# Performance work log

Hardware: AMD Instinct MI355X
Metric: run time of the kernel (lower is better)

Reference implementation:

```python
import jax, jax.numpy as jnp
import numpy as np

H = 1024      # hidden_size
V = 32000     # vocab_size
MAX_LEN = 32  # decode steps
B = 64        # batch


def _uni(key, shape, s):
    return jax.random.uniform(key, shape, jnp.float32, -s, s)


def setup_inputs() -> dict:
    key = jax.random.key(0)
    ks = jax.random.split(key, 10)
    s = 1.0 / np.sqrt(H)
    return {
        "vectors": jax.random.normal(ks[0], (B, H), jnp.float32),
        "W_fc_in": _uni(ks[1], (H, H), s),
        "b_fc_in": _uni(ks[2], (H,), s),
        "W_ih": _uni(ks[3], (3 * H, H), s),   # torch GRU weight_ih_l0 (r,z,n)
        "W_hh": _uni(ks[4], (3 * H, H), s),
        "b_ih": _uni(ks[5], (3 * H,), s),
        "b_hh": _uni(ks[6], (3 * H,), s),
        "W_out": _uni(ks[7], (V, H), s),
        "b_out": _uni(ks[8], (V,), s),
        "top_k": 8,
    }


def reference(vectors, W_fc_in, b_fc_in, W_ih, W_hh, b_ih, b_hh, W_out, b_out, top_k):
    # hidden = fc_in(vectors); initial GRU input is zeros
    h0 = vectors @ W_fc_in.T + b_fc_in           # [B, H]
    x0 = jnp.zeros_like(h0)

    def gru_cell(carry, _):
        h, x = carry
        gi = x @ W_ih.T + b_ih                   # [B, 3H]
        gh = h @ W_hh.T + b_hh                   # [B, 3H]
        i_r, i_z, i_n = jnp.split(gi, 3, axis=-1)
        h_r, h_z, h_n = jnp.split(gh, 3, axis=-1)
        r = jax.nn.sigmoid(i_r + h_r)
        z = jax.nn.sigmoid(i_z + h_z)
        n = jnp.tanh(i_n + r * h_n)
        h_new = (1.0 - z) * n + z * h            # PyTorch GRU update
        # out == h_new for single-layer GRU; inputs = out feeds back
        return (h_new, h_new), h_new

    _, outs = jax.lax.scan(gru_cell, (h0, x0), None, length=MAX_LEN)  # [T, B, H]

    # fc_out + log_softmax over vocab, for all steps at once
    logits = jnp.einsum('tbh,vh->tbv', outs, W_out) + b_out           # [T, B, V]
    logp = jax.nn.log_softmax(logits, axis=-1)

    # topk then multinomial over exp(top logp) == categorical over top logp
    top_p, top_i = jax.lax.top_k(logp, top_k)                         # [T, B, K]
    samp = jax.random.categorical(jax.random.key(42), top_p, axis=-1)  # [T, B]
    tokens = jnp.take_along_axis(top_i, samp[..., None], axis=-1)[..., 0]
    return tokens.T.astype(jnp.int32)                                  # [B, T]
```

## Files before the change

### kernel.cpp

```cpp
#include <hip/hip_runtime.h>
#include <stdint.h>

typedef unsigned int u32;
typedef unsigned long long u64;
typedef unsigned short ushort;
typedef __attribute__((ext_vector_type(8))) short bf16x8;
typedef __attribute__((ext_vector_type(4))) float f32x4;

#define JAX_PARTITIONABLE 1

#define HD     1024
#define BBATCH 64
#define TSTEP  32
#define VOCAB  32000
#define NROWS  2048
#define GATE6  6144
#define NCB    250
#define NCAND  16

__device__ __forceinline__ void threefry2x32(u32 k0, u32 k1, u32 x0, u32 x1,
                                             u32& y0, u32& y1) {
  u32 ks2 = k0 ^ k1 ^ 0x1BD11BDAu;
  x0 += k0; x1 += k1;
#define TFR(r) do { x0 += x1; x1 = (x1 << (r)) | (x1 >> (32 - (r))); x1 ^= x0; } while (0)
  TFR(13); TFR(15); TFR(26); TFR(6);   x0 += k1;  x1 += ks2 + 1u;
  TFR(17); TFR(29); TFR(16); TFR(24);  x0 += ks2; x1 += k0 + 2u;
  TFR(13); TFR(15); TFR(26); TFR(6);   x0 += k0;  x1 += k1 + 3u;
  TFR(17); TFR(29); TFR(16); TFR(24);  x0 += k1;  x1 += ks2 + 4u;
  TFR(13); TFR(15); TFR(26); TFR(6);   x0 += ks2; x1 += k0 + 5u;
#undef TFR
  y0 = x0; y1 = x1;
}

__device__ __forceinline__ u32 jax_random_bits(u32 n) {
#if JAX_PARTITIONABLE
  u32 y0, y1; threefry2x32(0u, 42u, 0u, n, y0, y1);
  return y0 ^ y1;
#else
  u32 y0, y1;
  if (n < 8192u) { threefry2x32(0u, 42u, n, n + 8192u, y0, y1); return y0; }
  else           { threefry2x32(0u, 42u, n - 8192u, n, y0, y1); return y1; }
#endif
}

__device__ __forceinline__ u64 packkey(float v, int idx) {
  u32 b = __float_as_uint(v);
  b = (b & 0x80000000u) ? ~b : (b | 0x80000000u);
  return ((u64)b << 32) | (u64)(~(u32)idx);
}

__device__ __forceinline__ void insert4(u64* t4, u64 k) {
  if (k > t4[3]) {
    t4[3] = k;
    if (t4[3] > t4[2]) { u64 tm = t4[2]; t4[2] = t4[3]; t4[3] = tm; }
    if (t4[2] > t4[1]) { u64 tm = t4[1]; t4[1] = t4[2]; t4[2] = tm; }
    if (t4[1] > t4[0]) { u64 tm = t4[0]; t4[0] = t4[1]; t4[1] = tm; }
  }
}

__device__ __forceinline__ ushort f2bf_rne(float x) {
  u32 u = __float_as_uint(x);
  return (ushort)((u + 0x7fffu + ((u >> 16) & 1u)) >> 16);
}
__device__ __forceinline__ float bf2f(ushort h) {
  return __uint_as_float(((u32)h) << 16);
}

typedef const __attribute__((address_space(1))) void* gas_ptr;
typedef __attribute__((address_space(3))) void* las_ptr;
__device__ __forceinline__ void gload16(const void* g, void* l) {
  __builtin_amdgcn_global_load_lds((gas_ptr)g, (las_ptr)l, 16, 0, 0);
}

__global__ __launch_bounds__(256) void tobf16(const float* __restrict__ src,
                                              ushort* __restrict__ dst, int n8) {
  int i = blockIdx.x * 256 + threadIdx.x;
  const int stride = gridDim.x * 256;
  for (; i < n8; i += stride) {
    const float4* s4 = (const float4*)src + (size_t)i * 2;
    float4 a = s4[0], b = s4[1];
    u32 o0 = f2bf_rne(a.x) | ((u32)f2bf_rne(a.y) << 16);
    u32 o1 = f2bf_rne(a.z) | ((u32)f2bf_rne(a.w) << 16);
    u32 o2 = f2bf_rne(b.x) | ((u32)f2bf_rne(b.y) << 16);
    u32 o3 = f2bf_rne(b.z) | ((u32)f2bf_rne(b.w) << 16);
    ((uint4*)dst)[i] = make_uint4(o0, o1, o2, o3);
  }
}

__global__ __launch_bounds__(256) void tobf16x3_gruP(
    const float* __restrict__ Wih, const float* __restrict__ Whh,
    ushort* __restrict__ w1, ushort* __restrict__ w2, ushort* __restrict__ w3) {
  int i = blockIdx.x * 256 + threadIdx.x;
  if (i >= GATE6 * (HD / 8)) return;
  int rp = i >> 7;
  int kc = i & 127;
  int b = rp / 48, rem = rp % 48;
  int g = rem >> 3, jp = rem & 7;
  const float* src = (g < 3)
      ? (Wih + ((size_t)g * HD + b * 8 + jp) * HD)
      : (Whh + ((size_t)(g - 3) * HD + b * 8 + jp) * HD);
  const float4* s4 = (const float4*)(src + kc * 8);
  float v[8];
  float4 a = s4[0], bb = s4[1];
  v[0]=a.x; v[1]=a.y; v[2]=a.z; v[3]=a.w; v[4]=bb.x; v[5]=bb.y; v[6]=bb.z; v[7]=bb.w;
  ushort p1[8], p2[8], p3[8];
#pragma unroll
  for (int e = 0; e < 8; ++e) {
    p1[e] = f2bf_rne(v[e]);
    float r1 = v[e] - bf2f(p1[e]);
    p2[e] = f2bf_rne(r1);
    float r2 = r1 - bf2f(p2[e]);
    p3[e] = f2bf_rne(r2);
  }
  u32 o1[4], o2[4], o3[4];
#pragma unroll
  for (int e = 0; e < 4; ++e) {
    o1[e] = p1[2*e] | ((u32)p1[2*e+1] << 16);
    o2[e] = p2[2*e] | ((u32)p2[2*e+1] << 16);
    o3[e] = p3[2*e] | ((u32)p3[2*e+1] << 16);
  }
  ((uint4*)w1)[i] = make_uint4(o1[0], o1[1], o1[2], o1[3]);
  ((uint4*)w2)[i] = make_uint4(o2[0], o2[1], o2[2], o2[3]);
  ((uint4*)w3)[i] = make_uint4(o3[0], o3[1], o3[2], o3[3]);
}

__global__ __launch_bounds__(256) void gemm64_nt(
    const float* __restrict__ A, const float* __restrict__ B,
    float* __restrict__ part) {
  __shared__ float4 As4[64 * 33];
  __shared__ float4 Bs4[32 * 33];
  const int tid = threadIdx.x;
  const int n0 = blockIdx.x * 32;
  const float* Brow = B + (size_t)n0 * HD;
  const int ks = blockIdx.y * 256;
  const int tc = tid & 7, trg = tid >> 3;
  float acc[2][4] = {};
  for (int kc = 0; kc < 2; ++kc) {
    const int k0 = ks + kc * 128;
#pragma unroll
    for (int l = 0; l < 8; ++l) {
      int m = tid + l * 256; int row = m >> 5, k4 = m & 31;
      As4[row * 33 + k4] = *(const float4*)(A + (size_t)row * HD + k0 + k4 * 4);
    }
#pragma unroll
    for (int l = 0; l < 4; ++l) {
      int m = tid + l * 256; int row = m >> 5, k4 = m & 31;
      Bs4[row * 33 + k4] = *(const float4*)(Brow + (size_t)row * HD + k0 + k4 * 4);
    }
    __syncthreads();
#pragma unroll
    for (int kq = 0; kq < 32; ++kq) {
      float4 av[2], bv[4];
      av[0] = As4[trg * 33 + kq];
      av[1] = As4[(trg + 32) * 33 + kq];
      bv[0] = Bs4[tc * 33 + kq];
      bv[1] = Bs4[(tc + 8) * 33 + kq];
      bv[2] = Bs4[(tc + 16) * 33 + kq];
      bv[3] = Bs4[(tc + 24) * 33 + kq];
#pragma unroll
      for (int i = 0; i < 2; ++i)
#pragma unroll
        for (int j = 0; j < 4; ++j) {
          acc[i][j] += av[i].x * bv[j].x;
          acc[i][j] += av[i].y * bv[j].y;
          acc[i][j] += av[i].z * bv[j].z;
          acc[i][j] += av[i].w * bv[j].w;
        }
    }
    __syncthreads();
  }
  float* P = part + (size_t)blockIdx.y * BBATCH * HD;
#pragma unroll
  for (int i = 0; i < 2; ++i) {
    int b = trg + 32 * i;
#pragma unroll
    for (int j = 0; j < 4; ++j)
      P[(size_t)b * HD + n0 + tc + 8 * j] = acc[i][j];
  }
}

__global__ __launch_bounds__(256) void combine_fcin(
    const float* __restrict__ part, const float* __restrict__ b_fc,
    float* __restrict__ h, ushort* __restrict__ h1, ushort* __restrict__ h2,
    ushort* __restrict__ h3) {
  int idx = blockIdx.x * 256 + threadIdx.x;
  int j = idx & 1023; int b = idx >> 10;
  const size_t S = (size_t)BBATCH * HD;
  const float* p = part + (size_t)b * HD;
  float d = p[j]; d += p[S + j]; d += p[2 * S + j]; d += p[3 * S + j];
  float hv = d + b_fc[j];
  h[idx] = hv;
  ushort a = f2bf_rne(hv);
  float r1 = hv - bf2f(a);
  ushort bb = f2bf_rne(r1);
  float r2 = r1 - bf2f(bb);
  h1[idx] = a; h2[idx] = bb; h3[idx] = f2bf_rne(r2);
}

__global__ __launch_bounds__(128) void gru_step(
    const ushort* __restrict__ W1, const ushort* __restrict__ W2,
    const ushort* __restrict__ W3,
    const float* __restrict__ b_ih, const float* __restrict__ b_hh,
    float* __restrict__ h, float* __restrict__ outs,
    ushort* __restrict__ outs_bf,
    ushort* __restrict__ h1, ushort* __restrict__ h2, ushort* __restrict__ h3,
    int t) {
  __shared__ ushort Bs[2][3][3072];
  const int tid = threadIdx.x;
  const int lane = tid & 63, w = tid >> 6;
  const int grp = blockIdx.x >> 4;
  const int rmd = blockIdx.x & 15;
  const int hb = rmd >> 3;
  const int b = grp * 8 + (rmd & 7);
  const ushort* B1g = W1 + (size_t)b * 48 * HD;
  const ushort* B2g = W2 + (size_t)b * 48 * HD;
  const ushort* B3g = W3 + (size_t)b * 48 * HD;
  const int rc = lane >> 3;
  const int gr8 = ((lane & 7) ^ rc) * 8;
  const int l15 = lane & 15;
  const int kc4 = lane >> 4;
  const int arow = hb * 32 + w * 16 + l15;

#define STAGE_B(buf, kt) do {                                         \
    const int k0_ = (kt) * 64;                                        \
    _Pragma("unroll")                                                 \
    for (int c_ = 0; c_ < 9; ++c_) {                                  \
      int q_ = w * 9 + c_;                                            \
      const ushort* src_; ushort* dst_;                               \
      if (q_ < 6)       { src_ = B1g + (size_t)(q_ * 8 + rc) * HD;    \
                          dst_ = &Bs[buf][0][q_ * 512]; }             \
      else if (q_ < 12) { src_ = B2g + (size_t)((q_ - 6) * 8 + rc) * HD; \
                          dst_ = &Bs[buf][1][(q_ - 6) * 512]; }       \
      else              { src_ = B3g + (size_t)((q_ - 12) * 8 + rc) * HD; \
                          dst_ = &Bs[buf][2][(q_ - 12) * 512]; }      \
      gload16(src_ + k0_ + gr8, dst_);                                \
    }                                                                 \
  } while (0)

#define LOAD_A(dst, kt) do {                                          \
    _Pragma("unroll")                                                 \
    for (int ks_ = 0; ks_ < 2; ++ks_) {                               \
      const int ke_ = (kt) * 64 + ks_ * 32 + kc4 * 8;                 \
      dst[ks_][0] = *(const bf16x8*)(h1 + (size_t)arow * HD + ke_);   \
      dst[ks_][1] = *(const bf16x8*)(h2 + (size_t)arow * HD + ke_);   \
      dst[ks_][2] = *(const bf16x8*)(h3 + (size_t)arow * HD + ke_);   \
    }                                                                 \
  } while (0)

#define COMPUTE_G(AR, buf) do {                                       \
    _Pragma("unroll")                                                 \
    for (int ks_ = 0; ks_ < 2; ++ks_) {                               \
      const int kb_ = ks_ * 64 + kc4 * 16;                            \
      bf16x8 b1_[3], b2_[3], b3_[3];                                  \
      _Pragma("unroll")                                               \
      for (int nt_ = 0; nt_ < 3; ++nt_) {                             \
        int br_ = nt_ * 16 + l15;                                     \
        int bo_ = br_ * 128 + (kb_ ^ ((br_ & 7) << 4));               \
        b1_[nt_] = *(const bf16x8*)((const char*)&Bs[buf][0][0] + bo_); \
        b2_[nt_] = *(const bf16x8*)((const char*)&Bs[buf][1][0] + bo_); \
        b3_[nt_] = *(const bf16x8*)((const char*)&Bs[buf][2][0] + bo_); \
      }                                                               \
      _Pragma("unroll")                                               \
      for (int nt_ = 0; nt_ < 3; ++nt_) {                             \
        acc[nt_] = __builtin_amdgcn_mfma_f32_16x16x32_bf16(AR[ks_][2], b1_[nt_], acc[nt_], 0, 0, 0); \
        acc[nt_] = __builtin_amdgcn_mfma_f32_16x16x32_bf16(AR[ks_][0], b3_[nt_], acc[nt_], 0, 0, 0); \
        acc[nt_] = __builtin_amdgcn_mfma_f32_16x16x32_bf16(AR[ks_][1], b2_[nt_], acc[nt_], 0, 0, 0); \
        acc[nt_] = __builtin_amdgcn_mfma_f32_16x16x32_bf16(AR[ks_][1], b1_[nt_], acc[nt_], 0, 0, 0); \
        acc[nt_] = __builtin_amdgcn_mfma_f32_16x16x32_bf16(AR[ks_][0], b2_[nt_], acc[nt_], 0, 0, 0); \
        acc[nt_] = __builtin_amdgcn_mfma_f32_16x16x32_bf16(AR[ks_][0], b1_[nt_], acc[nt_], 0, 0, 0); \
      }                                                               \
    }                                                                 \
  } while (0)

  f32x4 acc[3];
#pragma unroll
  for (int nt = 0; nt < 3; ++nt) acc[nt] = (f32x4){0.f, 0.f, 0.f, 0.f};

  bf16x8 aA[2][3], aB[2][3];
  LOAD_A(aA, 0); STAGE_B(0, 0);
  LOAD_A(aB, 1); STAGE_B(1, 1);

#pragma unroll
  for (int kt2 = 0; kt2 < 8; ++kt2) {
    const int kte = kt2 * 2, kto = kte + 1;
    asm volatile("s_waitcnt vmcnt(15)" ::: "memory");
    __builtin_amdgcn_s_barrier();
    __builtin_amdgcn_sched_barrier(0);
    COMPUTE_G(aA, 0);
    __builtin_amdgcn_sched_barrier(0);
    __builtin_amdgcn_s_barrier();
    if (kte + 2 < 16) { LOAD_A(aA, kte + 2); STAGE_B(0, kte + 2); }
    if (kto < 15) {
      asm volatile("s_waitcnt vmcnt(15)" ::: "memory");
    } else {
      asm volatile("s_waitcnt vmcnt(0)" ::: "memory");
    }
    __builtin_amdgcn_s_barrier();
    __builtin_amdgcn_sched_barrier(0);
    COMPUTE_G(aB, 1);
    __builtin_amdgcn_sched_barrier(0);
    __builtin_amdgcn_s_barrier();
    if (kto + 2 < 16) { LOAD_A(aB, kto + 2); STAGE_B(1, kto + 2); }
  }
#undef STAGE_B
#undef LOAD_A
#undef COMPUTE_G

  const bool low = (l15 < 8);
  const int j = b * 8 + l15;
  float bi_r = 0.f, bi_z = 0.f, bi_n = 0.f, bh_r = 0.f, bh_z = 0.f, bh_n = 0.f;
  if (low) {
    bi_r = b_ih[j]; bi_z = b_ih[HD + j]; bi_n = b_ih[2 * HD + j];
    bh_r = b_hh[j]; bh_z = b_hh[HD + j]; bh_n = b_hh[2 * HD + j];
  }
#pragma unroll
  for (int r = 0; r < 4; ++r) {
    float v0 = acc[0][r], v1 = acc[1][r], v2 = acc[2][r];
    float p0 = __shfl_xor(v0, 8);
    float p1 = __shfl_xor(v1, 8);
    float p2 = __shfl_xor(v2, 8);
    if (low) {
      float gir = (t == 0) ? bi_r : (v0 + bi_r);
      float giz = (t == 0) ? bi_z : (p0 + bi_z);
      float gin = (t == 0) ? bi_n : (v1 + bi_n);
      float ghr = p1 + bh_r;
      float ghz = v2 + bh_z;
      float ghn = p2 + bh_n;
      float rr = 1.0f / (1.0f + expf(-(gir + ghr)));
      float zz = 1.0f / (1.0f + expf(-(giz + ghz)));
      float nn = tanhf(gin + rr * ghn);
      int i = hb * 32 + w * 16 + (lane >> 4) * 4 + r;
      int idx = i * HD + j;
      float hp = h[idx];
      float hn2 = (1.0f - zz) * nn + zz * hp;
      h[idx] = hn2;
      size_t o = ((size_t)t * BBATCH + i) * HD + j;
      outs[o] = hn2;
      ushort a = f2bf_rne(hn2);
      outs_bf[o] = a;
      float r1 = hn2 - bf2f(a);
      ushort bb2 = f2bf_rne(r1);
      float r2 = r1 - bf2f(bb2);
      h1[idx] = a; h2[idx] = bb2; h3[idx] = f2bf_rne(r2);
    }
  }
}

__global__ __launch_bounds__(256) void gemm_out_mfma(
    const ushort* __restrict__ Abf, const ushort* __restrict__ Bbf,
    const float* __restrict__ b_out, u64* __restrict__ keys) {
  __shared__ ushort Sm[2][2][8192];
  float* Cs = (float*)&Sm[0][0][0];
  u64* pkL1 = (u64*)((char*)&Sm[0][0][0] + 17024);
  u64* pkL2 = pkL1 + 1024;

  const int tid = threadIdx.x;
  const int lane = tid & 63;
  const int wid = tid >> 6;
  const int wr = wid >> 1, wc = wid & 1;
  const int cb = blockIdx.y;
  const int n0 = cb * 128;
  const int r0 = blockIdx.x * 128;

  const ushort* Ag = Abf + (size_t)r0 * HD;
  const ushort* Bg = Bbf + (size_t)n0 * HD;
  const int rc = lane >> 3;
  const int gr8 = ((lane & 7) ^ rc) * 8;
  const int l15 = lane & 15;
  const int kseg = (lane >> 4) * 16;

#define STAGE_OUT(buf, kt) do {                                      \
    ushort* SA_ = &Sm[buf][0][0];                                    \
    ushort* SB_ = &Sm[buf][1][0];                                    \
    const int k0_ = (kt) * 64;                                       \
    _Pragma("unroll")                                                \
    for (int c_ = 0; c_ < 4; ++c_) {                                 \
      int ch_ = wid * 4 + c_;                                        \
      int row_ = ch_ * 8 + rc;                                       \
      gload16(Ag + (size_t)row_ * HD + k0_ + gr8, SA_ + ch_ * 512);  \
      gload16(Bg + (size_t)row_ * HD + k0_ + gr8, SB_ + ch_ * 512);  \
    }                                                                \
  } while (0)

#define COMPUTE_OUT(buf) do {                                        \
    const ushort* SA_ = &Sm[buf][0][0];                              \
    const ushort* SB_ = &Sm[buf][1][0];                              \
    _Pragma("unroll")                                                \
    for (int ks_ = 0; ks_ < 2; ++ks_) {                              \
      bf16x8 a_[4], b_[4];                                           \
      const int kb_ = ks_ * 64 + kseg;                               \
      _Pragma("unroll")                                              \
      for (int m_ = 0; m_ < 4; ++m_) {                               \
        int row_ = wr * 64 + m_ * 16 + l15;                          \
        int off_ = row_ * 128 + (kb_ ^ ((row_ & 7) << 4));           \
        a_[m_] = *(const bf16x8*)((const char*)SA_ + off_);          \
// ... 30 lines not shown
      STAGE_OUT(p ^ 1, kt + 1);
      asm volatile("s_waitcnt vmcnt(8)" ::: "memory");
    } else {
      asm volatile("s_waitcnt vmcnt(0)" ::: "memory");
    }
    __builtin_amdgcn_s_barrier();
    __builtin_amdgcn_sched_barrier(0);
    COMPUTE_OUT(p);
    __builtin_amdgcn_sched_barrier(0);
    __builtin_amdgcn_s_barrier();
    p ^= 1;
  }
  __syncthreads();

#pragma unroll
  for (int q = 0; q < 4; ++q) {
    if (wr == (q >> 1)) {
#pragma unroll
      for (int mi = 0; mi < 2; ++mi) {
        const int m = (q & 1) * 2 + mi;
#pragma unroll
        for (int n = 0; n < 4; ++n) {
          int c = wc * 64 + n * 16 + l15;
#pragma unroll
          for (int j = 0; j < 4; ++j) {
            int lr = mi * 16 + (lane >> 4) * 4 + j;
            Cs[lr * 133 + c] = acc[m][n][j] + bo[n];
          }
        }
      }
    }
    __syncthreads();
    {
      int rr = tid >> 3, seg = tid & 7;
      const float* rp = Cs + rr * 133 + seg * 16;
      u64 t4[4] = {0, 0, 0, 0};
#pragma unroll
      for (int c = 0; c < 16; ++c) insert4(t4, packkey(rp[c], n0 + seg * 16 + c));
      u64* d = pkL1 + (rr * 8 + seg) * 4;
      d[0] = t4[0]; d[1] = t4[1]; d[2] = t4[2]; d[3] = t4[3];
    }
    __syncthreads();
    if (tid < 64) {
      int rr = tid >> 1, hf = tid & 1;
      const u64* s = pkL1 + (rr * 8 + hf * 4) * 4;
      u64 t4[4] = {s[0], s[1], s[2], s[3]};
#pragma unroll
      for (int e = 4; e < 16; ++e) insert4(t4, s[e]);
      u64* d = pkL2 + tid * 4;
      d[0] = t4[0]; d[1] = t4[1]; d[2] = t4[2]; d[3] = t4[3];
    }
    __syncthreads();
    if (tid < 32) {
      const u64* s = pkL2 + tid * 8;
      u64 t4[4] = {s[0], s[1], s[2], s[3]};
      insert4(t4, s[4]); insert4(t4, s[5]); insert4(t4, s[6]); insert4(t4, s[7]);
      int grow = r0 + q * 32 + tid;
      u64* kp2 = keys + ((size_t)grow * NCB + cb) * 4;
      kp2[0] = t4[0]; kp2[1] = t4[1]; kp2[2] = t4[2]; kp2[3] = t4[3];
    }
    __syncthreads();
  }
#undef STAGE_OUT
#undef COMPUTE_OUT
}

__global__ __launch_bounds__(64) void merge_sample2(
// ... 87 lines not shown
      u32 bits = jax_random_bits((u32)(r * 8 + k));
      float f = __uint_as_float((bits >> 9) | 0x3f800000u) - 1.0f;
      float u = f * (1.0f - TINY) + TINY;
      u = fmaxf(TINY, u);
      float g = -logf(-logf(u));
      float s = g + lp;
      if (s > best) { best = s; bi = k; }
    }
    int t = r >> 6, b = r & 63;
    out[b * TSTEP + t] = vi[bi];
  }
}

extern "C" void kernel_launch(void* const* d_in, const int* in_sizes, int n_in,
                              void* d_out, int out_size, void* d_ws, size_t ws_size,
                              hipStream_t stream) {
  (void)in_sizes; (void)n_in; (void)out_size; (void)ws_size;
  const float* vectors = (const float*)d_in[0];
  const float* W_fc_in = (const float*)d_in[1];
  const float* b_fc_in = (const float*)d_in[2];
  const float* W_ih    = (const float*)d_in[3];
  const float* W_hh    = (const float*)d_in[4];
  const float* b_ih    = (const float*)d_in[5];
  const float* b_hh    = (const float*)d_in[6];
  const float* W_out   = (const float*)d_in[7];
  const float* b_out   = (const float*)d_in[8];
  int* out = (int*)d_out;

  char* w = (char*)d_ws;
  float* h = (float*)w;          w += (size_t)BBATCH * HD * 4;
  float* outs = (float*)w;       w += (size_t)NROWS * HD * 4;
  ushort* outs_bf = (ushort*)w;  w += (size_t)NROWS * HD * 2;
  ushort* Wbf = (ushort*)w;      w += (size_t)VOCAB * HD * 2;
  char* X = w;                   w += (size_t)3 * GATE6 * HD * 2;
  ushort* Wg1 = (ushort*)X;
  ushort* Wg2 = Wg1 + (size_t)GATE6 * HD;
  ushort* Wg3 = Wg2 + (size_t)GATE6 * HD;
  u64* keys = (u64*)X;
  ushort* h1 = (ushort*)w;       w += (size_t)BBATCH * HD * 2;
  ushort* h2 = (ushort*)w;       w += (size_t)BBATCH * HD * 2;
  ushort* h3 = (ushort*)w;       w += (size_t)BBATCH * HD * 2;
  float* part = (float*)w;

  tobf16<<<4096, 256, 0, stream>>>(W_out, Wbf, VOCAB * HD / 8);
  tobf16x3_gruP<<<GATE6 * (HD / 8) / 256, 256, 0, stream>>>(W_ih, W_hh,
                                                            Wg1, Wg2, Wg3);

  gemm64_nt<<<dim3(32, 4), 256, 0, stream>>>(vectors, W_fc_in, part);
  combine_fcin<<<256, 256, 0, stream>>>(part, b_fc_in, h, h1, h2, h3);

  for (int t = 0; t < TSTEP; ++t)
    gru_step<<<256, 128, 0, stream>>>(Wg1, Wg2, Wg3, b_ih, b_hh,
                                      h, outs, outs_bf, h1, h2, h3, t);

  gemm_out_mfma<<<dim3(16, NCB), 256, 0, stream>>>(outs_bf, Wbf, b_out, keys);

  merge_sample2<<<NROWS, 64, 0, stream>>>(keys, outs, W_out, b_out, out);
}
```

Measured before the change: 1.070 ms.

## Fuse GRU steps into one persistent kernel with LDS-resident weights and grid barrier

Replaces 32 per-step gru_step launches with a single persistent gru_all kernel of 256 blocks. Each block loads its 24-row slice of the three-way bf16-split gate weights into LDS once and keeps it there for all steps. Steps are synchronised with a hierarchical atomic grid barrier, and the bf16 hidden-state copies are double-buffered. This removes per-step launch overhead and the repeated re-streaming of weights from global memory. In exchange it depends on all 256 blocks being co-resident and on barrier correctness. It also swaps the thread-to-row/segment mapping in the output top-k reduction.

```diff
diff --git a/kernel.cpp b/kernel.cpp
--- a/kernel.cpp
+++ b/kernel.cpp
@@ -17,6 +17,7 @@
 #define GATE6  6144
 #define NCB    250
 #define NCAND  16
+#define GRUB   256
 
 __device__ __forceinline__ void threefry2x32(u32 k0, u32 k1, u32 x0, u32 x1,
                                              u32& y0, u32& y1) {
@@ -72,6 +73,36 @@
   __builtin_amdgcn_global_load_lds((gas_ptr)g, (las_ptr)l, 16, 0, 0);
 }
 
+__device__ __forceinline__ void grid_bar2(u32* B, int nPerGrp) {
+  __syncthreads();
+  if (threadIdx.x == 0) {
+    __threadfence();
+    const int g = blockIdx.x & 7;
+    u32* gc = B + g * 32;
+    u32* gg = B + 256 + g * 32;
+    u32 mygen = __hip_atomic_load(gg, __ATOMIC_RELAXED, __HIP_MEMORY_SCOPE_AGENT);
+    u32 a = __hip_atomic_fetch_add(gc, 1u, __ATOMIC_ACQ_REL, __HIP_MEMORY_SCOPE_AGENT);
+    if (a == (u32)nPerGrp - 1) {
+      __hip_atomic_store(gc, 0u, __ATOMIC_RELAXED, __HIP_MEMORY_SCOPE_AGENT);
+      u32* GC = B + 512; u32* GG = B + 544;
+      u32 mg = __hip_atomic_load(GG, __ATOMIC_RELAXED, __HIP_MEMORY_SCOPE_AGENT);
+      u32 ga = __hip_atomic_fetch_add(GC, 1u, __ATOMIC_ACQ_REL, __HIP_MEMORY_SCOPE_AGENT);
+      if (ga == 7u) {
+        __hip_atomic_store(GC, 0u, __ATOMIC_RELAXED, __HIP_MEMORY_SCOPE_AGENT);
+        __hip_atomic_fetch_add(GG, 1u, __ATOMIC_RELEASE, __HIP_MEMORY_SCOPE_AGENT);
+      } else {
+        while (__hip_atomic_load(GG, __ATOMIC_ACQUIRE, __HIP_MEMORY_SCOPE_AGENT) == mg)
+          __builtin_amdgcn_s_sleep(1);
+      }
+      __hip_atomic_fetch_add(gg, 1u, __ATOMIC_RELEASE, __HIP_MEMORY_SCOPE_AGENT);
+    } else {
+      while (__hip_atomic_load(gg, __ATOMIC_ACQUIRE, __HIP_MEMORY_SCOPE_AGENT) == mygen)
+        __builtin_amdgcn_s_sleep(1);
+    }
+  }
+  __syncthreads();
+}
+
 __global__ __launch_bounds__(256) void tobf16(const float* __restrict__ src,
                                               ushort* __restrict__ dst, int n8) {
   int i = blockIdx.x * 256 + threadIdx.x;
@@ -87,18 +118,18 @@
   }
 }
 
-__global__ __launch_bounds__(256) void tobf16x3_gruP(
+__global__ __launch_bounds__(256) void tobf16x3_gruP24(
     const float* __restrict__ Wih, const float* __restrict__ Whh,
     ushort* __restrict__ w1, ushort* __restrict__ w2, ushort* __restrict__ w3) {
   int i = blockIdx.x * 256 + threadIdx.x;
   if (i >= GATE6 * (HD / 8)) return;
   int rp = i >> 7;
   int kc = i & 127;
-  int b = rp / 48, rem = rp % 48;
-  int g = rem >> 3, jp = rem & 7;
+  int b = rp / 24, rem = rp % 24;
+  int g = rem >> 2, jp = rem & 3;
   const float* src = (g < 3)
-      ? (Wih + ((size_t)g * HD + b * 8 + jp) * HD)
-      : (Whh + ((size_t)(g - 3) * HD + b * 8 + jp) * HD);
+      ? (Wih + ((size_t)g * HD + b * 4 + jp) * HD)
+      : (Whh + ((size_t)(g - 3) * HD + b * 4 + jp) * HD);
   const float4* s4 = (const float4*)(src + kc * 8);
   float v[8];
   float4 a = s4[0], bb = s4[1];
@@ -197,151 +228,122 @@
   h1[idx] = a; h2[idx] = bb; h3[idx] = f2bf_rne(r2);
 }
 
-__global__ __launch_bounds__(128) void gru_step(
+__global__ __launch_bounds__(256, 1) void gru_all(
     const ushort* __restrict__ W1, const ushort* __restrict__ W2,
     const ushort* __restrict__ W3,
     const float* __restrict__ b_ih, const float* __restrict__ b_hh,
-    float* __restrict__ h, float* __restrict__ outs,
-    ushort* __restrict__ outs_bf,
-    ushort* __restrict__ h1, ushort* __restrict__ h2, ushort* __restrict__ h3,
-    int t) {
-  __shared__ ushort Bs[2][3][3072];
+    const float* __restrict__ h0,
+    float* __restrict__ outs, ushort* __restrict__ outs_bf,
+    ushort* __restrict__ hA1, ushort* __restrict__ hA2, ushort* __restrict__ hA3,
+    ushort* __restrict__ hB1, ushort* __restrict__ hB2, ushort* __restrict__ hB3,
+    u32* __restrict__ bar) {
+  __shared__ ushort S[76928];
+  float* Cg = (float*)(S + 73728);
   const int tid = threadIdx.x;
   const int lane = tid & 63, w = tid >> 6;
-  const int grp = blockIdx.x >> 4;
-  const int rmd = blockIdx.x & 15;
-  const int hb = rmd >> 3;
-  const int b = grp * 8 + (rmd & 7);
-  const ushort* B1g = W1 + (size_t)b * 48 * HD;
-  const ushort* B2g = W2 + (size_t)b * 48 * HD;
-  const ushort* B3g = W3 + (size_t)b * 48 * HD;
-  const int rc = lane >> 3;
-  const int gr8 = ((lane & 7) ^ rc) * 8;
-  const int l15 = lane & 15;
-  const int kc4 = lane >> 4;
-  const int arow = hb * 32 + w * 16 + l15;
-
-#define STAGE_B(buf, kt) do {                                         \
-    const int k0_ = (kt) * 64;                                        \
-    _Pragma("unroll")                                                 \
-    for (int c_ = 0; c_ < 9; ++c_) {                                  \
-      int q_ = w * 9 + c_;                                            \
-      const ushort* src_; ushort* dst_;                               \
-      if (q_ < 6)       { src_ = B1g + (size_t)(q_ * 8 + rc) * HD;    \
-                          dst_ = &Bs[buf][0][q_ * 512]; }             \
-      else if (q_ < 12) { src_ = B2g + (size_t)((q_ - 6) * 8 + rc) * HD; \
-                          dst_ = &Bs[buf][1][(q_ - 6) * 512]; }       \
-      else              { src_ = B3g + (size_t)((q_ - 12) * 8 + rc) * HD; \
-                          dst_ = &Bs[buf][2][(q_ - 12) * 512]; }      \
-      gload16(src_ + k0_ + gr8, dst_);                                \
-    }                                                                 \
-  } while (0)
-
-#define LOAD_A(dst, kt) do {                                          \
-    _Pragma("unroll")                                                 \
-    for (int ks_ = 0; ks_ < 2; ++ks_) {                               \
-      const int ke_ = (kt) * 64 + ks_ * 32 + kc4 * 8;                 \
-      dst[ks_][0] = *(const bf16x8*)(h1 + (size_t)arow * HD + ke_);   \
-      dst[ks_][1] = *(const bf16x8*)(h2 + (size_t)arow * HD + ke_);   \
-      dst[ks_][2] = *(const bf16x8*)(h3 + (size_t)arow * HD + ke_);   \
-    }                                                                 \
-  } while (0)
-
-#define COMPUTE_G(AR, buf) do {                                       \
-    _Pragma("unroll")                                                 \
-    for (int ks_ = 0; ks_ < 2; ++ks_) {                               \
-      const int kb_ = ks_ * 64 + kc4 * 16;                            \
-      bf16x8 b1_[3], b2_[3], b3_[3];                                  \
-      _Pragma("unroll")                                               \
-      for (int nt_ = 0; nt_ < 3; ++nt_) {                             \
-        int br_ = nt_ * 16 + l15;                                     \
-        int bo_ = br_ * 128 + (kb_ ^ ((br_ & 7) << 4));               \
-        b1_[nt_] = *(const bf16x8*)((const char*)&Bs[buf][0][0] + bo_); \
-        b2_[nt_] = *(const bf16x8*)((const char*)&Bs[buf][1][0] + bo_); \
-        b3_[nt_] = *(const bf16x8*)((const char*)&Bs[buf][2][0] + bo_); \
-      }                                                               \
-      _Pragma("unroll")                                               \
-      for (int nt_ = 0; nt_ < 3; ++nt_) {                             \
-        acc[nt_] = __builtin_amdgcn_mfma_f32_16x16x32_bf16(AR[ks_][2], b1_[nt_], acc[nt_], 0, 0, 0); \
-        acc[nt_] = __builtin_amdgcn_mfma_f32_16x16x32_bf16(AR[ks_][0], b3_[nt_], acc[nt_], 0, 0, 0); \
-        acc[nt_] = __builtin_amdgcn_mfma_f32_16x16x32_bf16(AR[ks_][1], b2_[nt_], acc[nt_], 0, 0, 0); \
-        acc[nt_] = __builtin_amdgcn_mfma_f32_16x16x32_bf16(AR[ks_][1], b1_[nt_], acc[nt_], 0, 0, 0); \
-        acc[nt_] = __builtin_amdgcn_mfma_f32_16x16x32_bf16(AR[ks_][0], b2_[nt_], acc[nt_], 0, 0, 0); \
-        acc[nt_] = __builtin_amdgcn_mfma_f32_16x16x32_bf16(AR[ks_][0], b1_[nt_], acc[nt_], 0, 0, 0); \
-      }                                                               \
-    }                                                                 \
-  } while (0)
-
-  f32x4 acc[3];
-#pragma unroll
-  for (int nt = 0; nt < 3; ++nt) acc[nt] = (f32x4){0.f, 0.f, 0.f, 0.f};
-
-  bf16x8 aA[2][3], aB[2][3];
-  LOAD_A(aA, 0); STAGE_B(0, 0);
-  LOAD_A(aB, 1); STAGE_B(1, 1);
-
-#pragma unroll
-  for (int kt2 = 0; kt2 < 8; ++kt2) {
-    const int kte = kt2 * 2, kto = kte + 1;
-    asm volatile("s_waitcnt vmcnt(15)" ::: "memory");
-    __builtin_amdgcn_s_barrier();
-    __builtin_amdgcn_sched_barrier(0);
-    COMPUTE_G(aA, 0);
-    __builtin_amdgcn_sched_barrier(0);
-    __builtin_amdgcn_s_barrier();
-    if (kte + 2 < 16) { LOAD_A(aA, kte + 2); STAGE_B(0, kte + 2); }
-    if (kto < 15) {
-      asm volatile("s_waitcnt vmcnt(15)" ::: "memory");
-    } else {
-      asm volatile("s_waitcnt vmcnt(0)" ::: "memory");
-    }
-    __builtin_amdgcn_s_barrier();
-    __builtin_amdgcn_sched_barrier(0);
-    COMPUTE_G(aB, 1);
-    __builtin_amdgcn_sched_barrier(0);
-    __builtin_amdgcn_s_barrier();
-    if (kto + 2 < 16) { LOAD_A(aB, kto + 2); STAGE_B(1, kto + 2); }
-  }
-#undef STAGE_B
-#undef LOAD_A
-#undef COMPUTE_G
-
-  const bool low = (l15 < 8);
-  const int j = b * 8 + l15;
-  float bi_r = 0.f, bi_z = 0.f, bi_n = 0.f, bh_r = 0.f, bh_z = 0.f, bh_n = 0.f;
-  if (low) {
-    bi_r = b_ih[j]; bi_z = b_ih[HD + j]; bi_n = b_ih[2 * HD + j];
-    bh_r = b_hh[j]; bh_z = b_hh[HD + j]; bh_n = b_hh[2 * HD + j];
-  }
-#pragma unroll
-  for (int r = 0; r < 4; ++r) {
-    float v0 = acc[0][r], v1 = acc[1][r], v2 = acc[2][r];
-    float p0 = __shfl_xor(v0, 8);
-    float p1 = __shfl_xor(v1, 8);
-    float p2 = __shfl_xor(v2, 8);
-    if (low) {
+  const int b = blockIdx.x;
+  const int l15 = lane & 15, kc4 = lane >> 4;
+
+  {
+    const ushort* Wl0 = W1 + (size_t)b * 24 * HD;
+    const ushort* Wl1 = W2 + (size_t)b * 24 * HD;
+    const ushort* Wl2 = W3 + (size_t)b * 24 * HD;
+#pragma unroll
+    for (int lv = 0; lv < 3; ++lv) {
+      const ushort* Wsrc = (lv == 0) ? Wl0 : (lv == 1) ? Wl1 : Wl2;
+      for (int k = 0; k < 12; ++k) {
+        int gi = w * 64 + k * 256 + lane;
+        int row = gi >> 7, gc = gi & 127;
+        gload16(Wsrc + (size_t)row * HD + ((gc ^ (row & 7)) * 8),
+                S + lv * 24576 + (w * 64 + k * 256) * 8);
+      }
+    }
+    asm volatile("s_waitcnt vmcnt(0)" ::: "memory");
+    __syncthreads();
+  }
+
+  const int gi_i = tid >> 2, gj = tid & 3;
+  const int jglob = b * 4 + gj;
+  float hreg = h0[gi_i * HD + jglob];
+  const float bi_r = b_ih[jglob], bi_z = b_ih[HD + jglob], bi_n = b_ih[2 * HD + jglob];
+  const float bh_r = b_hh[jglob], bh_z = b_hh[HD + jglob], bh_n = b_hh[2 * HD + jglob];
+  const int arow = w * 16 + l15;
+  const int q4 = lane >> 4;
+
+  for (int t = 0; t < TSTEP; ++t) {
+    const ushort* c1 = (t & 1) ? hB1 : hA1;
+    const ushort* c2 = (t & 1) ? hB2 : hA2;
+    const ushort* c3 = (t & 1) ? hB3 : hA3;
+    ushort* n1 = (t & 1) ? hA1 : hB1;
+    ushort* n2 = (t & 1) ? hA2 : hB2;
+    ushort* n3 = (t & 1) ? hA3 : hB3;
+
+    f32x4 acc[2];
+    acc[0] = (f32x4){0.f, 0.f, 0.f, 0.f};
+    acc[1] = (f32x4){0.f, 0.f, 0.f, 0.f};
+    const ushort* a1p = c1 + (size_t)arow * HD;
+    const ushort* a2p = c2 + (size_t)arow * HD;
+    const ushort* a3p = c3 + (size_t)arow * HD;
+#pragma unroll 8
+    for (int ks = 0; ks < 32; ++ks) {
+      const int ke = ks * 32 + kc4 * 8;
+      bf16x8 a1 = *(const bf16x8*)(a1p + ke);
+      bf16x8 a2 = *(const bf16x8*)(a2p + ke);
+      bf16x8 a3 = *(const bf16x8*)(a3p + ke);
+#pragma unroll
+      for (int nt = 0; nt < 2; ++nt) {
+        const int r = nt ? (16 + (l15 & 7)) : l15;
+        const int off = r * 2048 + ((ks * 64 + kc4 * 16) ^ ((r & 7) << 4));
+        bf16x8 b1 = *(const bf16x8*)((const char*)S + off);
+        bf16x8 b2 = *(const bf16x8*)((const char*)S + 49152 + off);
+        bf16x8 b3 = *(const bf16x8*)((const char*)S + 98304 + off);
+        acc[nt] = __builtin_amdgcn_mfma_f32_16x16x32_bf16(a3, b1, acc[nt], 0, 0, 0);
+        acc[nt] = __builtin_amdgcn_mfma_f32_16x16x32_bf16(a1, b3, acc[nt], 0, 0, 0);
+        acc[nt] = __builtin_amdgcn_mfma_f32_16x16x32_bf16(a2, b2, acc[nt], 0, 0, 0);
+        acc[nt] = __builtin_amdgcn_mfma_f32_16x16x32_bf16(a2, b1, acc[nt], 0, 0, 0);
+        acc[nt] = __builtin_amdgcn_mfma_f32_16x16x32_bf16(a1, b2, acc[nt], 0, 0, 0);
+        acc[nt] = __builtin_amdgcn_mfma_f32_16x16x32_bf16(a1, b1, acc[nt], 0, 0, 0);
+      }
+    }
+#pragma unroll
+    for (int j = 0; j < 4; ++j) {
+      int row = w * 16 + q4 * 4 + j;
+      Cg[row * 25 + l15] = acc[0][j];
+      if (l15 < 8) Cg[row * 25 + 16 + l15] = acc[1][j];
+    }
+    __syncthreads();
+
+    {
+      float v0 = Cg[gi_i * 25 + 0 + gj];
+      float v1 = Cg[gi_i * 25 + 4 + gj];
+      float v2 = Cg[gi_i * 25 + 8 + gj];
+      float v3 = Cg[gi_i * 25 + 12 + gj];
+      float v4 = Cg[gi_i * 25 + 16 + gj];
+      float v5 = Cg[gi_i * 25 + 20 + gj];
       float gir = (t == 0) ? bi_r : (v0 + bi_r);
-      float giz = (t == 0) ? bi_z : (p0 + bi_z);
-      float gin = (t == 0) ? bi_n : (v1 + bi_n);
-      float ghr = p1 + bh_r;
-      float ghz = v2 + bh_z;
-      float ghn = p2 + bh_n;
+      float giz = (t == 0) ? bi_z : (v1 + bi_z);
+      float gin = (t == 0) ? bi_n : (v2 + bi_n);
+      float ghr = v3 + bh_r;
+      float ghz = v4 + bh_z;
+      float ghn = v5 + bh_n;
       float rr = 1.0f / (1.0f + expf(-(gir + ghr)));
       float zz = 1.0f / (1.0f + expf(-(giz + ghz)));
       float nn = tanhf(gin + rr * ghn);
-      int i = hb * 32 + w * 16 + (lane >> 4) * 4 + r;
-      int idx = i * HD + j;
-      float hp = h[idx];
-      float hn2 = (1.0f - zz) * nn + zz * hp;
-      h[idx] = hn2;
-      size_t o = ((size_t)t * BBATCH + i) * HD + j;
+      float hn2 = (1.0f - zz) * nn + zz * hreg;
+      hreg = hn2;
+      size_t o = ((size_t)t * BBATCH + gi_i) * HD + jglob;
       outs[o] = hn2;
       ushort a = f2bf_rne(hn2);
       outs_bf[o] = a;
       float r1 = hn2 - bf2f(a);
       ushort bb2 = f2bf_rne(r1);
       float r2 = r1 - bf2f(bb2);
-      h1[idx] = a; h2[idx] = bb2; h3[idx] = f2bf_rne(r2);
+      int idx = gi_i * HD + jglob;
+      n1[idx] = a; n2[idx] = bb2; n3[idx] = f2bf_rne(r2);
+    }
+    if (t < TSTEP - 1) {
+      __threadfence();
+      grid_bar2(bar, GRUB / 8);
     }
   }
 }
@@ -457,7 +459,7 @@
     }
     __syncthreads();
     {
-      int rr = tid >> 3, seg = tid & 7;
+      int rr = tid & 31, seg = tid >> 5;
       const float* rp = Cs + rr * 133 + seg * 16;
       u64 t4[4] = {0, 0, 0, 0};
 #pragma unroll
@@ -616,21 +618,27 @@
   ushort* Wg2 = Wg1 + (size_t)GATE6 * HD;
   ushort* Wg3 = Wg2 + (size_t)GATE6 * HD;
   u64* keys = (u64*)X;
-  ushort* h1 = (ushort*)w;       w += (size_t)BBATCH * HD * 2;
-  ushort* h2 = (ushort*)w;       w += (size_t)BBATCH * HD * 2;
-  ushort* h3 = (ushort*)w;       w += (size_t)BBATCH * HD * 2;
+  ushort* hA1 = (ushort*)w;      w += (size_t)BBATCH * HD * 2;
+  ushort* hA2 = (ushort*)w;      w += (size_t)BBATCH * HD * 2;
+  ushort* hA3 = (ushort*)w;      w += (size_t)BBATCH * HD * 2;
+  ushort* hB1 = (ushort*)w;      w += (size_t)BBATCH * HD * 2;
+  ushort* hB2 = (ushort*)w;      w += (size_t)BBATCH * HD * 2;
+  ushort* hB3 = (ushort*)w;      w += (size_t)BBATCH * HD * 2;
+  u32* bar = (u32*)w;            w += 4096;
   float* part = (float*)w;
 
+  hipMemsetAsync(bar, 0, 4096, stream);
+
   tobf16<<<4096, 256, 0, stream>>>(W_out, Wbf, VOCAB * HD / 8);
-  tobf16x3_gruP<<<GATE6 * (HD / 8) / 256, 256, 0, stream>>>(W_ih, W_hh,
-                                                            Wg1, Wg2, Wg3);
+  tobf16x3_gruP24<<<GATE6 * (HD / 8) / 256, 256, 0, stream>>>(W_ih, W_hh,
+                                                              Wg1, Wg2, Wg3);
 
   gemm64_nt<<<dim3(32, 4), 256, 0, stream>>>(vectors, W_fc_in, part);
-  combine_fcin<<<256, 256, 0, stream>>>(part, b_fc_in, h, h1, h2, h3);
-
-  for (int t = 0; t < TSTEP; ++t)
-    gru_step<<<256, 128, 0, stream>>>(Wg1, Wg2, Wg3, b_ih, b_hh,
-                                      h, outs, outs_bf, h1, h2, h3, t);
+  combine_fcin<<<256, 256, 0, stream>>>(part, b_fc_in, h, hA1, hA2, hA3);
+
+  gru_all<<<GRUB, 256, 0, stream>>>(Wg1, Wg2, Wg3, b_ih, b_hh, h,
+                                    outs, outs_bf, hA1, hA2, hA3,
+                                    hB1, hB2, hB3, bar);
 
   gemm_out_mfma<<<dim3(16, NCB), 256, 0, stream>>>(outs_bf, Wbf, b_out, keys);
 
```

Result: slower. 2.517 ms (+135.2%).

## Replace 3-way bf16 split GRU GEMM with multi-level int8 MFMA decomposition

Applied to the files above, without the earlier changes.

The GRU weight and hidden-state split changes from three bf16 parts to four fixed-point int8 limbs, and the recurrent matmul now uses i32 16x16x64 int8 MFMAs that keep only the cross-limb products that matter. Weights are read straight from global memory, so the LDS staging and barriers go away, and the hidden state is double-buffered across steps to avoid read/write races. The output GEMM grid is also remapped so that a group of row-block tiles shares a vocab column block, with a tail fix, and the top-k reduction thread mapping is swapped. Risks are precision loss from the fixed-point scales, with h clamped to [-127/32, 127/32] at the top limb, and losing LDS reuse of the weights.

```diff
diff --git a/kernel.cpp b/kernel.cpp
--- a/kernel.cpp
+++ b/kernel.cpp
@@ -4,8 +4,10 @@
 typedef unsigned int u32;
 typedef unsigned long long u64;
 typedef unsigned short ushort;
+typedef signed char i8;
 typedef __attribute__((ext_vector_type(8))) short bf16x8;
 typedef __attribute__((ext_vector_type(4))) float f32x4;
+typedef __attribute__((ext_vector_type(4))) int i32x4;
 
 #define JAX_PARTITIONABLE 1
 
@@ -87,11 +89,12 @@
   }
 }
 
-__global__ __launch_bounds__(256) void tobf16x3_gruP(
+__global__ __launch_bounds__(256) void quantW_i8(
     const float* __restrict__ Wih, const float* __restrict__ Whh,
-    ushort* __restrict__ w1, ushort* __restrict__ w2, ushort* __restrict__ w3) {
+    i8* __restrict__ wq) {
   int i = blockIdx.x * 256 + threadIdx.x;
   if (i >= GATE6 * (HD / 8)) return;
+  const size_t WP = (size_t)GATE6 * HD;
   int rp = i >> 7;
   int kc = i & 127;
   int b = rp / 48, rem = rp % 48;
@@ -103,25 +106,26 @@
   float v[8];
   float4 a = s4[0], bb = s4[1];
   v[0]=a.x; v[1]=a.y; v[2]=a.z; v[3]=a.w; v[4]=bb.x; v[5]=bb.y; v[6]=bb.z; v[7]=bb.w;
-  ushort p1[8], p2[8], p3[8];
+  u64 p[4] = {0, 0, 0, 0};
 #pragma unroll
   for (int e = 0; e < 8; ++e) {
-    p1[e] = f2bf_rne(v[e]);
-    float r1 = v[e] - bf2f(p1[e]);
-    p2[e] = f2bf_rne(r1);
-    float r2 = r1 - bf2f(p2[e]);
-    p3[e] = f2bf_rne(r2);
-  }
-  u32 o1[4], o2[4], o3[4];
-#pragma unroll
-  for (int e = 0; e < 4; ++e) {
-    o1[e] = p1[2*e] | ((u32)p1[2*e+1] << 16);
-    o2[e] = p2[2*e] | ((u32)p2[2*e+1] << 16);
-    o3[e] = p3[2*e] | ((u32)p3[2*e+1] << 16);
-  }
-  ((uint4*)w1)[i] = make_uint4(o1[0], o1[1], o1[2], o1[3]);
-  ((uint4*)w2)[i] = make_uint4(o2[0], o2[1], o2[2], o2[3]);
-  ((uint4*)w3)[i] = make_uint4(o3[0], o3[1], o3[2], o3[3]);
+    float w0 = v[e];
+    float q1 = rintf(w0 * 0x1p11f);
+    float r1 = w0 - q1 * 0x1p-11f;
+    float q2 = rintf(r1 * 0x1p18f);
+    float r2 = r1 - q2 * 0x1p-18f;
+    float q3 = rintf(r2 * 0x1p25f);
+    float r3 = r2 - q3 * 0x1p-25f;
+    float q4 = rintf(r3 * 0x1p32f);
+    p[0] |= (u64)(u32)((int)q1 & 0xff) << (8 * e);
+    p[1] |= (u64)(u32)((int)q2 & 0xff) << (8 * e);
+    p[2] |= (u64)(u32)((int)q3 & 0xff) << (8 * e);
+    p[3] |= (u64)(u32)((int)q4 & 0xff) << (8 * e);
+  }
+  size_t off = (size_t)rp * HD + kc * 8;
+#pragma unroll
+  for (int lv = 0; lv < 4; ++lv)
+    *(u64*)(wq + lv * WP + off) = p[lv];
 }
 
 __global__ __launch_bounds__(256) void gemm64_nt(
@@ -179,10 +183,21 @@
   }
 }
 
+__device__ __forceinline__ void quant_h(float hv, i8* q) {
+  float q1 = rintf(hv * 0x1p5f);
+  q1 = fminf(fmaxf(q1, -127.f), 127.f);
+  float r1 = hv - q1 * 0x1p-5f;
+  float q2 = rintf(r1 * 0x1p12f);
+  float r2 = r1 - q2 * 0x1p-12f;
+  float q3 = rintf(r2 * 0x1p19f);
+  float r3 = r2 - q3 * 0x1p-19f;
+  float q4 = rintf(r3 * 0x1p26f);
+  q[0] = (i8)(int)q1; q[1] = (i8)(int)q2; q[2] = (i8)(int)q3; q[3] = (i8)(int)q4;
+}
+
 __global__ __launch_bounds__(256) void combine_fcin(
     const float* __restrict__ part, const float* __restrict__ b_fc,
-    float* __restrict__ h, ushort* __restrict__ h1, ushort* __restrict__ h2,
-    ushort* __restrict__ h3) {
+    float* __restrict__ h, i8* __restrict__ hq) {
   int idx = blockIdx.x * 256 + threadIdx.x;
   int j = idx & 1023; int b = idx >> 10;
   const size_t S = (size_t)BBATCH * HD;
@@ -190,121 +205,66 @@
   float d = p[j]; d += p[S + j]; d += p[2 * S + j]; d += p[3 * S + j];
   float hv = d + b_fc[j];
   h[idx] = hv;
-  ushort a = f2bf_rne(hv);
-  float r1 = hv - bf2f(a);
-  ushort bb = f2bf_rne(r1);
-  float r2 = r1 - bf2f(bb);
-  h1[idx] = a; h2[idx] = bb; h3[idx] = f2bf_rne(r2);
+  i8 q[4]; quant_h(hv, q);
+  const size_t HP = (size_t)BBATCH * HD;
+  hq[idx] = q[0]; hq[HP + idx] = q[1]; hq[2 * HP + idx] = q[2]; hq[3 * HP + idx] = q[3];
 }
 
 __global__ __launch_bounds__(128) void gru_step(
-    const ushort* __restrict__ W1, const ushort* __restrict__ W2,
-    const ushort* __restrict__ W3,
-    const float* __restrict__ b_ih, const float* __restrict__ b_hh,
-    float* __restrict__ h, float* __restrict__ outs,
-    ushort* __restrict__ outs_bf,
-    ushort* __restrict__ h1, ushort* __restrict__ h2, ushort* __restrict__ h3,
-    int t) {
-  __shared__ ushort Bs[2][3][3072];
+    const i8* __restrict__ Wq, const float* __restrict__ b_ih,
+    const float* __restrict__ b_hh, float* __restrict__ h,
+    float* __restrict__ outs, ushort* __restrict__ outs_bf,
+    const i8* __restrict__ hin, i8* __restrict__ hout, int t) {
   const int tid = threadIdx.x;
   const int lane = tid & 63, w = tid >> 6;
   const int grp = blockIdx.x >> 4;
   const int rmd = blockIdx.x & 15;
   const int hb = rmd >> 3;
   const int b = grp * 8 + (rmd & 7);
-  const ushort* B1g = W1 + (size_t)b * 48 * HD;
-  const ushort* B2g = W2 + (size_t)b * 48 * HD;
-  const ushort* B3g = W3 + (size_t)b * 48 * HD;
-  const int rc = lane >> 3;
-  const int gr8 = ((lane & 7) ^ rc) * 8;
-  const int l15 = lane & 15;
-  const int kc4 = lane >> 4;
+  const int l15 = lane & 15, kc4 = lane >> 4;
   const int arow = hb * 32 + w * 16 + l15;
 
-#define STAGE_B(buf, kt) do {                                         \
-    const int k0_ = (kt) * 64;                                        \
-    _Pragma("unroll")                                                 \
-    for (int c_ = 0; c_ < 9; ++c_) {                                  \
-      int q_ = w * 9 + c_;                                            \
-      const ushort* src_; ushort* dst_;                               \
-      if (q_ < 6)       { src_ = B1g + (size_t)(q_ * 8 + rc) * HD;    \
-                          dst_ = &Bs[buf][0][q_ * 512]; }             \
-      else if (q_ < 12) { src_ = B2g + (size_t)((q_ - 6) * 8 + rc) * HD; \
-                          dst_ = &Bs[buf][1][(q_ - 6) * 512]; }       \
-      else              { src_ = B3g + (size_t)((q_ - 12) * 8 + rc) * HD; \
-                          dst_ = &Bs[buf][2][(q_ - 12) * 512]; }      \
-      gload16(src_ + k0_ + gr8, dst_);                                \
-    }                                                                 \
-  } while (0)
-
-#define LOAD_A(dst, kt) do {                                          \
-    _Pragma("unroll")                                                 \
-    for (int ks_ = 0; ks_ < 2; ++ks_) {                               \
-      const int ke_ = (kt) * 64 + ks_ * 32 + kc4 * 8;                 \
-      dst[ks_][0] = *(const bf16x8*)(h1 + (size_t)arow * HD + ke_);   \
-      dst[ks_][1] = *(const bf16x8*)(h2 + (size_t)arow * HD + ke_);   \
-      dst[ks_][2] = *(const bf16x8*)(h3 + (size_t)arow * HD + ke_);   \
-    }                                                                 \
-  } while (0)
-
-#define COMPUTE_G(AR, buf) do {                                       \
-    _Pragma("unroll")                                                 \
-    for (int ks_ = 0; ks_ < 2; ++ks_) {                               \
-      const int kb_ = ks_ * 64 + kc4 * 16;                            \
-      bf16x8 b1_[3], b2_[3], b3_[3];                                  \
-      _Pragma("unroll")                                               \
-      for (int nt_ = 0; nt_ < 3; ++nt_) {                             \
-        int br_ = nt_ * 16 + l15;                                     \
-        int bo_ = br_ * 128 + (kb_ ^ ((br_ & 7) << 4));               \
-        b1_[nt_] = *(const bf16x8*)((const char*)&Bs[buf][0][0] + bo_); \
-        b2_[nt_] = *(const bf16x8*)((const char*)&Bs[buf][1][0] + bo_); \
-        b3_[nt_] = *(const bf16x8*)((const char*)&Bs[buf][2][0] + bo_); \
-      }                                                               \
-      _Pragma("unroll")                                               \
-      for (int nt_ = 0; nt_ < 3; ++nt_) {                             \
-        acc[nt_] = __builtin_amdgcn_mfma_f32_16x16x32_bf16(AR[ks_][2], b1_[nt_], acc[nt_], 0, 0, 0); \
-        acc[nt_] = __builtin_amdgcn_mfma_f32_16x16x32_bf16(AR[ks_][0], b3_[nt_], acc[nt_], 0, 0, 0); \
-        acc[nt_] = __builtin_amdgcn_mfma_f32_16x16x32_bf16(AR[ks_][1], b2_[nt_], acc[nt_], 0, 0, 0); \
-        acc[nt_] = __builtin_amdgcn_mfma_f32_16x16x32_bf16(AR[ks_][1], b1_[nt_], acc[nt_], 0, 0, 0); \
-        acc[nt_] = __builtin_amdgcn_mfma_f32_16x16x32_bf16(AR[ks_][0], b2_[nt_], acc[nt_], 0, 0, 0); \
-        acc[nt_] = __builtin_amdgcn_mfma_f32_16x16x32_bf16(AR[ks_][0], b1_[nt_], acc[nt_], 0, 0, 0); \
-      }                                                               \
-    }                                                                 \
-  } while (0)
-
-  f32x4 acc[3];
-#pragma unroll
-  for (int nt = 0; nt < 3; ++nt) acc[nt] = (f32x4){0.f, 0.f, 0.f, 0.f};
-
-  bf16x8 aA[2][3], aB[2][3];
-  LOAD_A(aA, 0); STAGE_B(0, 0);
-  LOAD_A(aB, 1); STAGE_B(1, 1);
-
-#pragma unroll
-  for (int kt2 = 0; kt2 < 8; ++kt2) {
-    const int kte = kt2 * 2, kto = kte + 1;
-    asm volatile("s_waitcnt vmcnt(15)" ::: "memory");
-    __builtin_amdgcn_s_barrier();
-    __builtin_amdgcn_sched_barrier(0);
-    COMPUTE_G(aA, 0);
-    __builtin_amdgcn_sched_barrier(0);
-    __builtin_amdgcn_s_barrier();
-    if (kte + 2 < 16) { LOAD_A(aA, kte + 2); STAGE_B(0, kte + 2); }
-    if (kto < 15) {
-      asm volatile("s_waitcnt vmcnt(15)" ::: "memory");
-    } else {
-      asm volatile("s_waitcnt vmcnt(0)" ::: "memory");
-    }
-    __builtin_amdgcn_s_barrier();
-    __builtin_amdgcn_sched_barrier(0);
-    COMPUTE_G(aB, 1);
-    __builtin_amdgcn_sched_barrier(0);
-    __builtin_amdgcn_s_barrier();
-    if (kto + 2 < 16) { LOAD_A(aB, kto + 2); STAGE_B(1, kto + 2); }
-  }
-#undef STAGE_B
-#undef LOAD_A
-#undef COMPUTE_G
+  const size_t WP = (size_t)GATE6 * HD;
+  const size_t HP = (size_t)BBATCH * HD;
+  const i8* Wb = Wq + (size_t)b * 48 * HD;
+  const i8* hrow = hin + (size_t)arow * HD;
+
+  i32x4 acc[6][3];
+#pragma unroll
+  for (int g = 0; g < 6; ++g)
+#pragma unroll
+    for (int nt = 0; nt < 3; ++nt) acc[g][nt] = (i32x4){0, 0, 0, 0};
+
+#pragma unroll 4
+  for (int kt = 0; kt < 16; ++kt) {
+    const int ko = kt * 64 + kc4 * 16;
+    i32x4 ha[4];
+#pragma unroll
+    for (int lv = 0; lv < 4; ++lv)
+      ha[lv] = *(const i32x4*)(hrow + lv * HP + ko);
+    i32x4 wb[4][3];
+#pragma unroll
+    for (int lv = 0; lv < 4; ++lv)
+#pragma unroll
+      for (int nt = 0; nt < 3; ++nt)
+        wb[lv][nt] = *(const i32x4*)(Wb + lv * WP + (size_t)(nt * 16 + l15) * HD + ko);
+#pragma unroll
+    for (int nt = 0; nt < 3; ++nt) {
+      acc[0][nt] = __builtin_amdgcn_mfma_i32_16x16x64_i8(ha[0], wb[0][nt], acc[0][nt], 0, 0, 0);
+      acc[1][nt] = __builtin_amdgcn_mfma_i32_16x16x64_i8(ha[0], wb[1][nt], acc[1][nt], 0, 0, 0);
+      acc[2][nt] = __builtin_amdgcn_mfma_i32_16x16x64_i8(ha[1], wb[0][nt], acc[2][nt], 0, 0, 0);
+      acc[3][nt] = __builtin_amdgcn_mfma_i32_16x16x64_i8(ha[0], wb[2][nt], acc[3][nt], 0, 0, 0);
+      acc[3][nt] = __builtin_amdgcn_mfma_i32_16x16x64_i8(ha[1], wb[1][nt], acc[3][nt], 0, 0, 0);
+      acc[3][nt] = __builtin_amdgcn_mfma_i32_16x16x64_i8(ha[2], wb[0][nt], acc[3][nt], 0, 0, 0);
+      acc[4][nt] = __builtin_amdgcn_mfma_i32_16x16x64_i8(ha[0], wb[3][nt], acc[4][nt], 0, 0, 0);
+      acc[4][nt] = __builtin_amdgcn_mfma_i32_16x16x64_i8(ha[1], wb[2][nt], acc[4][nt], 0, 0, 0);
+      acc[4][nt] = __builtin_amdgcn_mfma_i32_16x16x64_i8(ha[2], wb[1][nt], acc[4][nt], 0, 0, 0);
+      acc[4][nt] = __builtin_amdgcn_mfma_i32_16x16x64_i8(ha[3], wb[0][nt], acc[4][nt], 0, 0, 0);
+      acc[5][nt] = __builtin_amdgcn_mfma_i32_16x16x64_i8(ha[1], wb[3][nt], acc[5][nt], 0, 0, 0);
+      acc[5][nt] = __builtin_amdgcn_mfma_i32_16x16x64_i8(ha[2], wb[2][nt], acc[5][nt], 0, 0, 0);
+      acc[5][nt] = __builtin_amdgcn_mfma_i32_16x16x64_i8(ha[3], wb[1][nt], acc[5][nt], 0, 0, 0);
+    }
+  }
 
   const bool low = (l15 < 8);
   const int j = b * 8 + l15;
@@ -315,33 +275,41 @@
   }
 #pragma unroll
   for (int r = 0; r < 4; ++r) {
-    float v0 = acc[0][r], v1 = acc[1][r], v2 = acc[2][r];
-    float p0 = __shfl_xor(v0, 8);
-    float p1 = __shfl_xor(v1, 8);
-    float p2 = __shfl_xor(v2, 8);
+    float c[3];
+#pragma unroll
+    for (int nt = 0; nt < 3; ++nt) {
+      float v = (float)acc[5][nt][r] * 0x1p-44f;
+      v += (float)acc[4][nt][r] * 0x1p-37f;
+      v += (float)acc[3][nt][r] * 0x1p-30f;
+      v += (float)acc[2][nt][r] * 0x1p-23f;
+      v += (float)acc[1][nt][r] * 0x1p-23f;
+      v += (float)acc[0][nt][r] * 0x1p-16f;
+      c[nt] = v;
+    }
+    float p0 = __shfl_xor(c[0], 8);
+    float p1 = __shfl_xor(c[1], 8);
+    float p2 = __shfl_xor(c[2], 8);
     if (low) {
-      float gir = (t == 0) ? bi_r : (v0 + bi_r);
+      float gir = (t == 0) ? bi_r : (c[0] + bi_r);
       float giz = (t == 0) ? bi_z : (p0 + bi_z);
-      float gin = (t == 0) ? bi_n : (v1 + bi_n);
+      float gin = (t == 0) ? bi_n : (c[1] + bi_n);
       float ghr = p1 + bh_r;
-      float ghz = v2 + bh_z;
+      float ghz = c[2] + bh_z;
       float ghn = p2 + bh_n;
       float rr = 1.0f / (1.0f + expf(-(gir + ghr)));
       float zz = 1.0f / (1.0f + expf(-(giz + ghz)));
       float nn = tanhf(gin + rr * ghn);
-      int i = hb * 32 + w * 16 + (lane >> 4) * 4 + r;
+      int i = hb * 32 + w * 16 + kc4 * 4 + r;
       int idx = i * HD + j;
       float hp = h[idx];
       float hn2 = (1.0f - zz) * nn + zz * hp;
       h[idx] = hn2;
       size_t o = ((size_t)t * BBATCH + i) * HD + j;
       outs[o] = hn2;
-      ushort a = f2bf_rne(hn2);
-      outs_bf[o] = a;
-      float r1 = hn2 - bf2f(a);
-      ushort bb2 = f2bf_rne(r1);
-      float r2 = r1 - bf2f(bb2);
-      h1[idx] = a; h2[idx] = bb2; h3[idx] = f2bf_rne(r2);
+      outs_bf[o] = f2bf_rne(hn2);
+      i8 q[4]; quant_h(hn2, q);
+      hout[idx] = q[0]; hout[HP + idx] = q[1];
+      hout[2 * HP + idx] = q[2]; hout[3 * HP + idx] = q[3];
     }
   }
 }
@@ -358,9 +326,13 @@
   const int lane = tid & 63;
   const int wid = tid >> 6;
   const int wr = wid >> 1, wc = wid & 1;
-  const int cb = blockIdx.y;
+
+  int X = blockIdx.x, K = blockIdx.y;
+  if (X >= 2 && K >= 496) { int e = (X - 2) * 4 + (K - 496); X = e / 12; K = 500 + e % 12; }
+  const int cb = (K >> 4) * 8 + X;
+  const int rb = K & 15;
   const int n0 = cb * 128;
-  const int r0 = blockIdx.x * 128;
+  const int r0 = rb * 128;
 
   const ushort* Ag = Abf + (size_t)r0 * HD;
   const ushort* Bg = Bbf + (size_t)n0 * HD;
@@ -457,7 +429,7 @@
     }
     __syncthreads();
     {
-      int rr = tid >> 3, seg = tid & 7;
+      int rr = tid & 31, seg = tid >> 5;
       const float* rp = Cs + rr * 133 + seg * 16;
       u64 t4[4] = {0, 0, 0, 0};
 #pragma unroll
@@ -611,28 +583,27 @@
   float* outs = (float*)w;       w += (size_t)NROWS * HD * 4;
   ushort* outs_bf = (ushort*)w;  w += (size_t)NROWS * HD * 2;
   ushort* Wbf = (ushort*)w;      w += (size_t)VOCAB * HD * 2;
-  char* X = w;                   w += (size_t)3 * GATE6 * HD * 2;
-  ushort* Wg1 = (ushort*)X;
-  ushort* Wg2 = Wg1 + (size_t)GATE6 * HD;
-  ushort* Wg3 = Wg2 + (size_t)GATE6 * HD;
+  char* X = w;                   w += (size_t)4 * GATE6 * HD;
+  i8* Wq = (i8*)X;
   u64* keys = (u64*)X;
-  ushort* h1 = (ushort*)w;       w += (size_t)BBATCH * HD * 2;
-  ushort* h2 = (ushort*)w;       w += (size_t)BBATCH * HD * 2;
-  ushort* h3 = (ushort*)w;       w += (size_t)BBATCH * HD * 2;
+  i8* hQA = (i8*)w;              w += (size_t)4 * BBATCH * HD;
+  i8* hQB = (i8*)w;              w += (size_t)4 * BBATCH * HD;
   float* part = (float*)w;
 
   tobf16<<<4096, 256, 0, stream>>>(W_out, Wbf, VOCAB * HD / 8);
-  tobf16x3_gruP<<<GATE6 * (HD / 8) / 256, 256, 0, stream>>>(W_ih, W_hh,
-                                                            Wg1, Wg2, Wg3);
+  quantW_i8<<<GATE6 * (HD / 8) / 256, 256, 0, stream>>>(W_ih, W_hh, Wq);
 
   gemm64_nt<<<dim3(32, 4), 256, 0, stream>>>(vectors, W_fc_in, part);
-  combine_fcin<<<256, 256, 0, stream>>>(part, b_fc_in, h, h1, h2, h3);
-
-  for (int t = 0; t < TSTEP; ++t)
-    gru_step<<<256, 128, 0, stream>>>(Wg1, Wg2, Wg3, b_ih, b_hh,
-                                      h, outs, outs_bf, h1, h2, h3, t);
-
-  gemm_out_mfma<<<dim3(16, NCB), 256, 0, stream>>>(outs_bf, Wbf, b_out, keys);
+  combine_fcin<<<256, 256, 0, stream>>>(part, b_fc_in, h, hQA);
+
+  for (int t = 0; t < TSTEP; ++t) {
+    const i8* hin = (t & 1) ? hQB : hQA;
+    i8* hout = (t & 1) ? hQA : hQB;
+    gru_step<<<256, 128, 0, stream>>>(Wq, b_ih, b_hh, h, outs, outs_bf,
+                                      hin, hout, t);
+  }
+
+  gemm_out_mfma<<<dim3(8, 500), 256, 0, stream>>>(outs_bf, Wbf, b_out, keys);
 
   merge_sample2<<<NROWS, 64, 0, stream>>>(keys, outs, W_out, b_out, out);
 }
```

Result: faster. 1.023 ms (-4.4%).
